# Performance work log

Hardware: AMD Instinct MI355X
Metric: run time of the kernel (lower is better)

## Reference

```python
import jax, jax.numpy as jnp
import numpy as np

N_NODES = 10000
N_EDGES = 160000
D = 42          # node_input_dim == node_hidden_dim
DE = 10         # edge_input_dim
DEH = 42        # edge_hidden_dim
N_STEPS = 6


def setup_inputs() -> dict:
    key = jax.random.key(0)
    ks = jax.random.split(key, 16)
    s = 0.1
    return {
        "n_feat": jax.random.normal(ks[0], (N_NODES, D), jnp.float32),
        "e_feat": jax.random.normal(ks[1], (N_EDGES, DE), jnp.float32),
        "src": jax.random.randint(ks[2], (N_EDGES,), 0, N_NODES),
        "dst": jax.random.randint(ks[3], (N_EDGES,), 0, N_NODES),
        # lin0: node_input_dim -> node_hidden_dim
        "lin0_w": s * jax.random.normal(ks[4], (D, D), jnp.float32),
        "lin0_b": s * jax.random.normal(ks[5], (D,), jnp.float32),
        # message_layer: hidden -> hidden
        "msg_w": s * jax.random.normal(ks[6], (D, D), jnp.float32),
        "msg_b": s * jax.random.normal(ks[7], (D,), jnp.float32),
        # edge_network: Linear(10,42) -> ReLU -> Linear(42, 42*42)
        "en_w1": s * jax.random.normal(ks[8], (DE, DEH), jnp.float32),
        "en_b1": s * jax.random.normal(ks[9], (DEH,), jnp.float32),
        "en_w2": s * jax.random.normal(ks[10], (DEH, D * D), jnp.float32),
        "en_b2": s * jax.random.normal(ks[11], (D * D,), jnp.float32),
        # NNConv bias (DGL NNConv has bias=True by default)
        "conv_b": s * jax.random.normal(ks[12], (D,), jnp.float32),
    }


def reference(n_feat, e_feat, src, dst,
              lin0_w, lin0_b, msg_w, msg_b,
              en_w1, en_b1, en_w2, en_b2, conv_b):
    N, d = n_feat.shape
    init = n_feat
    out = jax.nn.relu(n_feat @ lin0_w + lin0_b)                      # [N, d]
    # Per-edge weight matrices from edge features (e_feat is constant
    # across steps, so the edge MLP is hoisted out of the loop).
    w_edge = (jax.nn.relu(e_feat @ en_w1 + en_b1) @ en_w2 + en_b2)   # [E, d*d]
    w_edge = w_edge.reshape(-1, d, d)                                # [E, d_in, d_out]
    for _ in range(N_STEPS):
        # NNConv: gather src feats, per-edge matvec, scatter-sum to dst
        msgs = jnp.einsum('ei,eio->eo', out[src], w_edge)            # [E, d]
        agg = jax.ops.segment_sum(msgs, dst, num_segments=N)         # [N, d]
        # residual (in==out -> identity res_fc) + bias, then outer ReLU
        m = jax.nn.relu(agg + out + conv_b)
        out = jax.nn.relu(m @ msg_w + msg_b)
    return out + init
```

## Files before the change

### kernel.cpp

```cpp
#include <hip/hip_runtime.h>
#include <hip/hip_bf16.h>


#define N_NODES 10000
#define N_EDGES 160000
#define NCHK 5000
#define D 42
#define DE 10
#define XSTR 48
#define KI 1806
#define NKSTEP 57
#define SSTR 1832

typedef __attribute__((ext_vector_type(8))) short short8;
typedef __attribute__((ext_vector_type(4))) float f32x4;

__global__ __launch_bounds__(256) void k_lin0(const float* __restrict__ nf,
        const float* __restrict__ w, const float* __restrict__ b,
        __hip_bfloat16* __restrict__ out16) {
    int idx = blockIdx.x * 256 + threadIdx.x;
    if (idx >= N_NODES * XSTR) return;
    int n = idx / XSTR, j = idx % XSTR;
    float v = 0.f;
    if (j < D) {
        const float* row = nf + n * D;
        float acc = b[j];
        #pragma unroll
        for (int i = 0; i < D; ++i) acc = fmaf(row[i], w[i * D + j], acc);
        v = fmaxf(acc, 0.f);
    }
    out16[idx] = __float2bfloat16(v);
}

__global__ __launch_bounds__(256) void k_T2B(const float* __restrict__ w2,
        const float* __restrict__ b2, __hip_bfloat16* __restrict__ Bfr) {
    int idx = blockIdx.x * 256 + threadIdx.x;
    if (idx >= 3 * NKSTEP * 64 * 8) return;
    int j = idx & 7, lane = (idx >> 3) & 63;
    int ks = (idx >> 9) % NKSTEP, nt = idx / (NKSTEP * 512);
    int col = nt * 16 + (lane & 15);
    int k = ks * 32 + ((lane >> 4) * 8) + j;
    float v = 0.f;
    if (col < D && k < KI) {
        int kk = k / D, ii = k % D;
        v = (kk < D) ? w2[kk * (D * D) + ii * D + col] : b2[ii * D + col];
    }
    Bfr[idx] = __float2bfloat16(v);
}

__global__ __launch_bounds__(256) void k_hist(const int* __restrict__ dst,
        int* __restrict__ cnt) {
    int e = blockIdx.x * 256 + threadIdx.x;
    if (e < N_EDGES) atomicAdd(&cnt[dst[e]], 1);
}

__global__ __launch_bounds__(1024) void k_scan(const int* __restrict__ cnt,
        int* __restrict__ row_ptr, int* __restrict__ cursor) {
    __shared__ int buf[1024];
    __shared__ int s_run;
    const int t = threadIdx.x;
    if (t == 0) s_run = 0;
    __syncthreads();
    for (int base = 0; base < N_NODES; base += 1024) {
        int v = (base + t < N_NODES) ? cnt[base + t] : 0;
        buf[t] = v;
        __syncthreads();
        for (int off = 1; off < 1024; off <<= 1) {
            int add = (t >= off) ? buf[t - off] : 0;
            __syncthreads();
            buf[t] += add;
            __syncthreads();
        }
        int excl = buf[t] - v;
        if (base + t < N_NODES) {
            int val = s_run + excl;
            row_ptr[base + t] = val;
            cursor[base + t]  = val;
        }
        __syncthreads();
        if (t == 0) s_run += buf[1023];
        __syncthreads();
    }
    if (t == 0) { row_ptr[N_NODES] = s_run; cursor[N_NODES] = s_run; }
}

__global__ __launch_bounds__(256) void k_scatter(const int* __restrict__ dst,
        const int* __restrict__ src, int* __restrict__ cursor,
        int* __restrict__ srcp, int* __restrict__ eperm) {
    int e = blockIdx.x * 256 + threadIdx.x;
    if (e < N_EDGES) {
        int p = atomicAdd(&cursor[dst[e]], 1);
        srcp[p] = src[e];
        eperm[p] = e;
    }
}

__global__ __launch_bounds__(256) void k_hT(const float* __restrict__ ef,
        const float* __restrict__ w1, const float* __restrict__ b1,
        const int* __restrict__ eperm, __hip_bfloat16* __restrict__ hpT) {
    const int c = blockIdx.x;
    const int t = threadIdx.x;
    for (int j = t; j < 48 * 32; j += 256) {
        int k = j >> 5, ep = j & 31;
        int e = eperm[c * 32 + ep];
        float v;
        if (k < D) {
            const float* row = ef + (size_t)e * DE;
            float acc = b1[k];
            #pragma unroll
            for (int i = 0; i < DE; ++i) acc = fmaf(row[i], w1[i * D + k], acc);
            v = fmaxf(acc, 0.f);
        } else {
            v = (k == D) ? 1.0f : 0.f;
        }
        hpT[(size_t)c * 1536 + j] = __float2bfloat16(v);
    }
}

#define MFMA(A, B, C) C = __builtin_amdgcn_mfma_f32_16x16x32_bf16(A, B, C, 0, 0, 0)

__global__ __launch_bounds__(256) void k_step3(
        const __hip_bfloat16* __restrict__ hpT,
        const __hip_bfloat16* __restrict__ out_in,
        const int* __restrict__ srcp, const int* __restrict__ row_ptr,
        const __hip_bfloat16* __restrict__ Bfr,
        const float* __restrict__ nf, const float* __restrict__ msg_w,
        const float* __restrict__ msg_b, const float* __restrict__ conv_b,
        __hip_bfloat16* __restrict__ out16_dst, float* __restrict__ fout,
        int last) {
    __shared__ __align__(16) __hip_bfloat16 sS[8 * SSTR];
    __shared__ float sR[8 * 48];
    __shared__ float sM[8 * 48];
    const int t = threadIdx.x;
    const int wv = t >> 6;
    const int l = t & 63;
    const int g = l >> 4;
    const int g8 = g * 8;
    const int cl = l & 15;
    const int n0 = blockIdx.x * 8;
    const short* hpTs = (const short*)hpT;
    const short* xs = (const short*)out_in;

    for (int i = t; i < 8 * 48; i += 256) sR[i] = 0.f;
    for (int i = t; i < 8 * 18; i += 256)
        sS[(i / 18) * SSTR + KI + (i % 18)] = __float2bfloat16(0.f);

    const int nodeA = n0 + wv * 2, nodeB = nodeA + 1;
    const int begA = row_ptr[nodeA], endA = row_ptr[nodeA + 1];
    const int begB = endA, endB = row_ptr[nodeB + 1];
    const int c0A = begA >> 5, ncA = (endA > begA) ? ((endA - 1) >> 5) - c0A + 1 : 0;
    const int c0B = begB >> 5, ncB = (endB > begB) ? ((endB - 1) >> 5) - c0B + 1 : 0;
    const int ncmax = max(ncA, ncB);

    f32x4 cA[9], cB[9];
    #pragma unroll
    for (int i = 0; i < 9; ++i) { cA[i] = {0.f,0.f,0.f,0.f}; cB[i] = cA[i]; }

    for (int ci = 0; ci < ncmax; ++ci) {
        short8 aA0, aA1, aA2, bA0, bA1, bA2;
        short8 aB0, aB1, aB2, bB0, bB1, bB2;
        bool doA = ci < ncA, doB = ci < ncB;
        if (doA) {
            const int c = c0A + ci, c32 = c << 5;
            const short* hb = hpTs + (size_t)c * 1536 + cl * 32 + g8;
            aA0 = *(const short8*)(hb);
            aA1 = *(const short8*)(hb + 16 * 32);
            aA2 = *(const short8*)(hb + 32 * 32);
            int4 s0 = *(const int4*)(srcp + c32 + g8);
            int4 s1 = *(const int4*)(srcp + c32 + g8 + 4);
            const int se[8] = {s0.x, s0.y, s0.z, s0.w, s1.x, s1.y, s1.z, s1.w};
            #pragma unroll
            for (int j = 0; j < 8; ++j) {
                const short* xr = xs + (size_t)se[j] * XSTR + cl;
                bA0[j] = xr[0]; bA1[j] = xr[16]; bA2[j] = xr[32];
            }
            if (c32 < begA || c32 + 32 > endA) {
                #pragma unroll
                for (int j = 0; j < 8; ++j) {
                    int ep = c32 + g8 + j;
                    if (ep < begA || ep >= endA) { aA0[j] = 0; aA1[j] = 0; aA2[j] = 0; }
                }
            }
        }
        if (doB) {
            const int c = c0B + ci, c32 = c << 5;
            const short* hb = hpTs + (size_t)c * 1536 + cl * 32 + g8;
            aB0 = *(const short8*)(hb);
            aB1 = *(const short8*)(hb + 16 * 32);
            aB2 = *(const short8*)(hb + 32 * 32);
            int4 s0 = *(const int4*)(srcp + c32 + g8);
            int4 s1 = *(const int4*)(srcp + c32 + g8 + 4);
            const int se[8] = {s0.x, s0.y, s0.z, s0.w, s1.x, s1.y, s1.z, s1.w};
            #pragma unroll
            for (int j = 0; j < 8; ++j) {
                const short* xr = xs + (size_t)se[j] * XSTR + cl;
                bB0[j] = xr[0]; bB1[j] = xr[16]; bB2[j] = xr[32];
            }
            if (c32 < begB || c32 + 32 > endB) {
                #pragma unroll
                for (int j = 0; j < 8; ++j) {
                    int ep = c32 + g8 + j;
                    if (ep < begB || ep >= endB) { aB0[j] = 0; aB1[j] = 0; aB2[j] = 0; }
                }
            }
        }
        if (doA) {
            MFMA(aA0, bA0, cA[0]); MFMA(aA0, bA1, cA[1]); MFMA(aA0, bA2, cA[2]);
            MFMA(aA1, bA0, cA[3]); MFMA(aA1, bA1, cA[4]); MFMA(aA1, bA2, cA[5]);
            MFMA(aA2, bA0, cA[6]); MFMA(aA2, bA1, cA[7]); MFMA(aA2, bA2, cA[8]);
        }
        if (doB) {
            MFMA(aB0, bB0, cB[0]); MFMA(aB0, bB1, cB[1]); MFMA(aB0, bB2, cB[2]);
            MFMA(aB1, bB0, cB[3]); MFMA(aB1, bB1, cB[4]); MFMA(aB1, bB2, cB[5]);
            MFMA(aB2, bB0, cB[6]); MFMA(aB2, bB1, cB[7]); MFMA(aB2, bB2, cB[8]);
        }
    }
    #define ST(CC, NLOC, MT, NT)                                             \
        _Pragma("unroll")                                                    \
        for (int r = 0; r < 4; ++r) {                                        \
            int m = (MT) * 16 + g * 4 + r;                                   \
            int col = (NT) * 16 + cl;                                        \
            if (m < 43 && col < D)                                           \
                sS[(NLOC) * SSTR + m * D + col] = __float2bfloat16(CC[r]);   \
        }
    {
        const int nlA = wv * 2, nlB = nlA + 1;
        ST(cA[0], nlA, 0, 0) ST(cA[1], nlA, 0, 1) ST(cA[2], nlA, 0, 2)
        ST(cA[3], nlA, 1, 0) ST(cA[4], nlA, 1, 1) ST(cA[5], nlA, 1, 2)
        ST(cA[6], nlA, 2, 0) ST(cA[7], nlA, 2, 1) ST(cA[8], nlA, 2, 2)
        ST(cB[0], nlB, 0, 0) ST(cB[1], nlB, 0, 1) ST(cB[2], nlB, 0, 2)
        ST(cB[3], nlB, 1, 0) ST(cB[4], nlB, 1, 1) ST(cB[5], nlB, 1, 2)
        ST(cB[6], nlB, 2, 0) ST(cB[7], nlB, 2, 1) ST(cB[8], nlB, 2, 2)
    }
    #undef ST
    __syncthreads();

    {
        const int ks0 = (wv == 0) ? 0 : (wv * 14 + 1);
        const int ks1 = wv * 14 + 15;
        f32x4 d0 = {0.f,0.f,0.f,0.f}, d1 = d0, d2 = d0;
        const short* sSrow = (const short*)sS + (cl & 7) * SSTR + g8;
        const short* bb = (const short*)Bfr + (size_t)l * 8;
        for (int ks = ks0; ks < ks1; ++ks) {
            short8 a  = *(const short8*)(sSrow + ks * 32);
            short8 B0 = *(const short8*)(bb + (size_t)(0 * NKSTEP + ks) * 512);
            short8 B1 = *(const short8*)(bb + (size_t)(1 * NKSTEP + ks) * 512);
            short8 B2 = *(const short8*)(bb + (size_t)(2 * NKSTEP + ks) * 512);
            MFMA(a, B0, d0); MFMA(a, B1, d1); MFMA(a, B2, d2);
        }
        if (g < 2) {
            const int rl = g * 4;
            #pragma unroll
            for (int r = 0; r < 4; ++r) {
                atomicAdd(&sR[(rl + r) * 48 + cl],      d0[r]);
                atomicAdd(&sR[(rl + r) * 48 + 16 + cl], d1[r]);
                atomicAdd(&sR[(rl + r) * 48 + 32 + cl], d2[r]);
            }
        }
    }
    __syncthreads();

    float* sW = (float*)sS;
    for (int i = t; i < D * D; i += 256) sW[i] = msg_w[i];
    for (int idx = t; idx < 8 * 48; idx += 256) {
        int nl_ = idx / 48, o = idx % 48;
        float mv = 0.f;
        if (o < D) {
            float res = __bfloat162float(out_in[(size_t)(n0 + nl_) * XSTR + o]);
            mv = fmaxf(sR[idx] + res + conv_b[o], 0.f);
        }
        sM[idx] = mv;
    }
    __syncthreads();

    for (int idx = t; idx < 8 * 48; idx += 256) {
        int nl_ = idx / 48, pcol = idx % 48;
        if (pcol < D) {
            float s = msg_b[pcol];
            #pragma unroll 6
            for (int o = 0; o < D; ++o)
                s = fmaf(sM[nl_ * 48 + o], sW[o * D + pcol], s);
            float v = fmaxf(s, 0.f);
            if (last) {
                fout[(size_t)(n0 + nl_) * D + pcol] =
                    v + nf[(size_t)(n0 + nl_) * D + pcol];
            } else {
                out16_dst[(size_t)(n0 + nl_) * XSTR + pcol] = __float2bfloat16(v);
            }
        } else if (!last) {
            out16_dst[(size_t)(n0 + nl_) * XSTR + pcol] = __float2bfloat16(0.f);
        }
    }
}

extern "C" void kernel_launch(void* const* d_in, const int* in_sizes, int n_in,
                              void* d_out, int out_size, void* d_ws, size_t ws_size,
                              hipStream_t stream) {
    const float* nf    = (const float*)d_in[0];
    const float* ef    = (const float*)d_in[1];
    const int*   src   = (const int*)d_in[2];
    const int*   dst   = (const int*)d_in[3];
    const float* lin0w = (const float*)d_in[4];
    const float* lin0b = (const float*)d_in[5];
    const float* msgw  = (const float*)d_in[6];
    const float* msgb  = (const float*)d_in[7];
    const float* enw1  = (const float*)d_in[8];
    const float* enb1  = (const float*)d_in[9];
    const float* enw2  = (const float*)d_in[10];
    const float* enb2  = (const float*)d_in[11];
    const float* convb = (const float*)d_in[12];

    char* p = (char*)d_ws;
    auto alloc = [&](size_t bytes) -> char* {
        char* r = p; p += (bytes + 255) & ~(size_t)255; return r;
    };
    __hip_bfloat16* outA = (__hip_bfloat16*)alloc((size_t)N_NODES * XSTR * 2);
    __hip_bfloat16* outB = (__hip_bfloat16*)alloc((size_t)N_NODES * XSTR * 2);
    __hip_bfloat16* hpT  = (__hip_bfloat16*)alloc((size_t)NCHK * 1536 * 2);
    __hip_bfloat16* Bfr  = (__hip_bfloat16*)alloc((size_t)3 * NKSTEP * 64 * 8 * 2);
    int* cnt    = (int*)alloc((N_NODES + 1) * 4);
    int* rowp   = (int*)alloc((N_NODES + 1) * 4);
    int* cur    = (int*)alloc((N_NODES + 1) * 4);
    int* srcp   = (int*)alloc((size_t)N_EDGES * 4);
    int* eperm  = (int*)alloc((size_t)N_EDGES * 4);

    hipMemsetAsync(cnt, 0, (N_NODES + 1) * 4, stream);
    k_lin0<<<(N_NODES * XSTR + 255) / 256, 256, 0, stream>>>(nf, lin0w, lin0b, outA);
    k_T2B<<<(3 * NKSTEP * 64 * 8 + 255) / 256, 256, 0, stream>>>(enw2, enb2, Bfr);
    k_hist<<<(N_EDGES + 255) / 256, 256, 0, stream>>>(dst, cnt);
    k_scan<<<1, 1024, 0, stream>>>(cnt, rowp, cur);
    k_scatter<<<(N_EDGES + 255) / 256, 256, 0, stream>>>(dst, src, cur, srcp, eperm);
    k_hT<<<NCHK, 256, 0, stream>>>(ef, enw1, enb1, eperm, hpT);

    const int tiles = N_NODES / 8;
    __hip_bfloat16* bufs[2] = {outA, outB};
    for (int s_i = 0; s_i < 6; ++s_i) {
        const __hip_bfloat16* cin = bufs[s_i % 2];
        __hip_bfloat16* cout = bufs[(s_i + 1) % 2];
        int last = (s_i == 5) ? 1 : 0;
        k_step3<<<tiles, 256, 0, stream>>>(hpT, cin, srcp, rowp, Bfr,
                                           nf, msgw, msgb, convb,
                                           cout, (float*)d_out, last);
    }
}
```

Before: 357.9 us.

## Pre-gather source features into transposed chunk layout and enlarge node tiles

Adds a per-step k_gx kernel that gathers source-node features by edge order into a chunked transposed bf16 buffer (xeT), so the main step kernel loads B operands with contiguous vector loads instead of per-element scattered gathers. The step kernel now uses 512 threads and 16 nodes per block, handles one node at a time per wave with software prefetch of the next chunk, and uses all 16 MFMA rows in the second contraction. This trades an extra kernel launch and an extra round trip through global memory each step for coalesced loads and better MFMA utilisation.

```diff
diff --git a/kernel.cpp b/kernel.cpp
--- a/kernel.cpp
+++ b/kernel.cpp
@@ -117,129 +117,123 @@
     }
 }
 
+__global__ __launch_bounds__(256) void k_gx(
+        const __hip_bfloat16* __restrict__ x16, const int* __restrict__ srcp,
+        __hip_bfloat16* __restrict__ xeT) {
+    __shared__ short sx[128][50];
+    const int t = threadIdx.x;
+    const int base = blockIdx.x * 128;
+    const short* xs = (const short*)x16;
+    for (int idx = t; idx < 128 * 6; idx += 256) {
+        int el = idx / 6, cs = idx % 6;
+        int sp = srcp[base + el];
+        *(short8*)&sx[el][cs * 8] = *(const short8*)(xs + (size_t)sp * XSTR + cs * 8);
+    }
+    __syncthreads();
+    short* out = (short*)xeT + (size_t)blockIdx.x * 4 * 1536;
+    for (int idx = t; idx < 768; idx += 256) {
+        int cc = idx / 192, rem = idx % 192, row = rem >> 2, h8 = rem & 3;
+        short8 v;
+        #pragma unroll
+        for (int j = 0; j < 8; ++j) v[j] = sx[cc * 32 + h8 * 8 + j][row];
+        *(short8*)(out + (size_t)cc * 1536 + row * 32 + h8 * 8) = v;
+    }
+}
+
 #define MFMA(A, B, C) C = __builtin_amdgcn_mfma_f32_16x16x32_bf16(A, B, C, 0, 0, 0)
 
-__global__ __launch_bounds__(256) void k_step3(
+__global__ __launch_bounds__(512, 4) void k_step4(
         const __hip_bfloat16* __restrict__ hpT,
+        const __hip_bfloat16* __restrict__ xeT,
         const __hip_bfloat16* __restrict__ out_in,
-        const int* __restrict__ srcp, const int* __restrict__ row_ptr,
+        const int* __restrict__ row_ptr,
         const __hip_bfloat16* __restrict__ Bfr,
         const float* __restrict__ nf, const float* __restrict__ msg_w,
         const float* __restrict__ msg_b, const float* __restrict__ conv_b,
         __hip_bfloat16* __restrict__ out16_dst, float* __restrict__ fout,
         int last) {
-    __shared__ __align__(16) __hip_bfloat16 sS[8 * SSTR];
-    __shared__ float sR[8 * 48];
-    __shared__ float sM[8 * 48];
+    __shared__ __align__(16) __hip_bfloat16 sS[16 * SSTR];
+    __shared__ float sR[16 * 48];
+    __shared__ float sM[16 * 48];
     const int t = threadIdx.x;
     const int wv = t >> 6;
     const int l = t & 63;
     const int g = l >> 4;
     const int g8 = g * 8;
     const int cl = l & 15;
-    const int n0 = blockIdx.x * 8;
+    const int n0 = blockIdx.x * 16;
     const short* hpTs = (const short*)hpT;
-    const short* xs = (const short*)out_in;
-
-    for (int i = t; i < 8 * 48; i += 256) sR[i] = 0.f;
-    for (int i = t; i < 8 * 18; i += 256)
+    const short* xeTs = (const short*)xeT;
+
+    for (int i = t; i < 16 * 48; i += 512) sR[i] = 0.f;
+    for (int i = t; i < 16 * 18; i += 512)
         sS[(i / 18) * SSTR + KI + (i % 18)] = __float2bfloat16(0.f);
 
-    const int nodeA = n0 + wv * 2, nodeB = nodeA + 1;
-    const int begA = row_ptr[nodeA], endA = row_ptr[nodeA + 1];
-    const int begB = endA, endB = row_ptr[nodeB + 1];
-    const int c0A = begA >> 5, ncA = (endA > begA) ? ((endA - 1) >> 5) - c0A + 1 : 0;
-    const int c0B = begB >> 5, ncB = (endB > begB) ? ((endB - 1) >> 5) - c0B + 1 : 0;
-    const int ncmax = max(ncA, ncB);
-
-    f32x4 cA[9], cB[9];
-    #pragma unroll
-    for (int i = 0; i < 9; ++i) { cA[i] = {0.f,0.f,0.f,0.f}; cB[i] = cA[i]; }
-
-    for (int ci = 0; ci < ncmax; ++ci) {
-        short8 aA0, aA1, aA2, bA0, bA1, bA2;
-        short8 aB0, aB1, aB2, bB0, bB1, bB2;
-        bool doA = ci < ncA, doB = ci < ncB;
-        if (doA) {
-            const int c = c0A + ci, c32 = c << 5;
-            const short* hb = hpTs + (size_t)c * 1536 + cl * 32 + g8;
-            aA0 = *(const short8*)(hb);
-            aA1 = *(const short8*)(hb + 16 * 32);
-            aA2 = *(const short8*)(hb + 32 * 32);
-            int4 s0 = *(const int4*)(srcp + c32 + g8);
-            int4 s1 = *(const int4*)(srcp + c32 + g8 + 4);
-            const int se[8] = {s0.x, s0.y, s0.z, s0.w, s1.x, s1.y, s1.z, s1.w};
-            #pragma unroll
-            for (int j = 0; j < 8; ++j) {
-                const short* xr = xs + (size_t)se[j] * XSTR + cl;
-                bA0[j] = xr[0]; bA1[j] = xr[16]; bA2[j] = xr[32];
+    for (int q = 0; q < 2; ++q) {
+        const int nloc = wv * 2 + q;
+        const int node = n0 + nloc;
+        const int beg = row_ptr[node], end = row_ptr[node + 1];
+        const int c0 = beg >> 5;
+        const int nc = (end > beg) ? ((end - 1) >> 5) - c0 + 1 : 0;
+
+        f32x4 cc[9];
+        #pragma unroll
+        for (int i = 0; i < 9; ++i) cc[i] = {0.f, 0.f, 0.f, 0.f};
+
+        short8 a0, a1, a2, b0, b1, b2;
+        if (nc > 0) {
+            const size_t hb = (size_t)c0 * 1536 + cl * 32 + g8;
+            a0 = *(const short8*)(hpTs + hb);
+            a1 = *(const short8*)(hpTs + hb + 512);
+            a2 = *(const short8*)(hpTs + hb + 1024);
+            b0 = *(const short8*)(xeTs + hb);
+            b1 = *(const short8*)(xeTs + hb + 512);
+            b2 = *(const short8*)(xeTs + hb + 1024);
+        }
+        for (int ci = 0; ci < nc; ++ci) {
+            short8 na0, na1, na2, nb0, nb1, nb2;
+            if (ci + 1 < nc) {
+                const size_t hb = (size_t)(c0 + ci + 1) * 1536 + cl * 32 + g8;
+                na0 = *(const short8*)(hpTs + hb);
+                na1 = *(const short8*)(hpTs + hb + 512);
+                na2 = *(const short8*)(hpTs + hb + 1024);
+                nb0 = *(const short8*)(xeTs + hb);
+                nb1 = *(const short8*)(xeTs + hb + 512);
+                nb2 = *(const short8*)(xeTs + hb + 1024);
             }
-            if (c32 < begA || c32 + 32 > endA) {
+            const int c32 = (c0 + ci) << 5;
+            if (c32 < beg || c32 + 32 > end) {
                 #pragma unroll
                 for (int j = 0; j < 8; ++j) {
                     int ep = c32 + g8 + j;
-                    if (ep < begA || ep >= endA) { aA0[j] = 0; aA1[j] = 0; aA2[j] = 0; }
+                    if (ep < beg || ep >= end) { a0[j] = 0; a1[j] = 0; a2[j] = 0; }
                 }
             }
-        }
-        if (doB) {
-            const int c = c0B + ci, c32 = c << 5;
-            const short* hb = hpTs + (size_t)c * 1536 + cl * 32 + g8;
-            aB0 = *(const short8*)(hb);
-            aB1 = *(const short8*)(hb + 16 * 32);
-            aB2 = *(const short8*)(hb + 32 * 32);
-            int4 s0 = *(const int4*)(srcp + c32 + g8);
-            int4 s1 = *(const int4*)(srcp + c32 + g8 + 4);
-            const int se[8] = {s0.x, s0.y, s0.z, s0.w, s1.x, s1.y, s1.z, s1.w};
-            #pragma unroll
-            for (int j = 0; j < 8; ++j) {
-                const short* xr = xs + (size_t)se[j] * XSTR + cl;
-                bB0[j] = xr[0]; bB1[j] = xr[16]; bB2[j] = xr[32];
+            MFMA(a0, b0, cc[0]); MFMA(a0, b1, cc[1]); MFMA(a0, b2, cc[2]);
+            MFMA(a1, b0, cc[3]); MFMA(a1, b1, cc[4]); MFMA(a1, b2, cc[5]);
+            MFMA(a2, b0, cc[6]); MFMA(a2, b1, cc[7]); MFMA(a2, b2, cc[8]);
+            a0 = na0; a1 = na1; a2 = na2; b0 = nb0; b1 = nb1; b2 = nb2;
+        }
+        #define ST(CI, MT, NT)                                               \
+            _Pragma("unroll")                                                \
+            for (int r = 0; r < 4; ++r) {                                    \
+                int m = (MT) * 16 + g * 4 + r;                               \
+                int col = (NT) * 16 + cl;                                    \
+                if (m < 43 && col < D)                                       \
+                    sS[nloc * SSTR + m * D + col] = __float2bfloat16(cc[CI][r]); \
             }
-            if (c32 < begB || c32 + 32 > endB) {
-                #pragma unroll
-                for (int j = 0; j < 8; ++j) {
-                    int ep = c32 + g8 + j;
-                    if (ep < begB || ep >= endB) { aB0[j] = 0; aB1[j] = 0; aB2[j] = 0; }
-                }
-            }
-        }
-        if (doA) {
-            MFMA(aA0, bA0, cA[0]); MFMA(aA0, bA1, cA[1]); MFMA(aA0, bA2, cA[2]);
-            MFMA(aA1, bA0, cA[3]); MFMA(aA1, bA1, cA[4]); MFMA(aA1, bA2, cA[5]);
-            MFMA(aA2, bA0, cA[6]); MFMA(aA2, bA1, cA[7]); MFMA(aA2, bA2, cA[8]);
-        }
-        if (doB) {
-            MFMA(aB0, bB0, cB[0]); MFMA(aB0, bB1, cB[1]); MFMA(aB0, bB2, cB[2]);
-            MFMA(aB1, bB0, cB[3]); MFMA(aB1, bB1, cB[4]); MFMA(aB1, bB2, cB[5]);
-            MFMA(aB2, bB0, cB[6]); MFMA(aB2, bB1, cB[7]); MFMA(aB2, bB2, cB[8]);
-        }
-    }
-    #define ST(CC, NLOC, MT, NT)                                             \
-        _Pragma("unroll")                                                    \
-        for (int r = 0; r < 4; ++r) {                                        \
-            int m = (MT) * 16 + g * 4 + r;                                   \
-            int col = (NT) * 16 + cl;                                        \
-            if (m < 43 && col < D)                                           \
-                sS[(NLOC) * SSTR + m * D + col] = __float2bfloat16(CC[r]);   \
-        }
+        ST(0, 0, 0) ST(1, 0, 1) ST(2, 0, 2)
+        ST(3, 1, 0) ST(4, 1, 1) ST(5, 1, 2)
+        ST(6, 2, 0) ST(7, 2, 1) ST(8, 2, 2)
+        #undef ST
+    }
+    __syncthreads();
+
     {
-        const int nlA = wv * 2, nlB = nlA + 1;
-        ST(cA[0], nlA, 0, 0) ST(cA[1], nlA, 0, 1) ST(cA[2], nlA, 0, 2)
-        ST(cA[3], nlA, 1, 0) ST(cA[4], nlA, 1, 1) ST(cA[5], nlA, 1, 2)
-        ST(cA[6], nlA, 2, 0) ST(cA[7], nlA, 2, 1) ST(cA[8], nlA, 2, 2)
-        ST(cB[0], nlB, 0, 0) ST(cB[1], nlB, 0, 1) ST(cB[2], nlB, 0, 2)
-        ST(cB[3], nlB, 1, 0) ST(cB[4], nlB, 1, 1) ST(cB[5], nlB, 1, 2)
-        ST(cB[6], nlB, 2, 0) ST(cB[7], nlB, 2, 1) ST(cB[8], nlB, 2, 2)
-    }
-    #undef ST
-    __syncthreads();
-
-    {
-        const int ks0 = (wv == 0) ? 0 : (wv * 14 + 1);
-        const int ks1 = wv * 14 + 15;
-        f32x4 d0 = {0.f,0.f,0.f,0.f}, d1 = d0, d2 = d0;
-        const short* sSrow = (const short*)sS + (cl & 7) * SSTR + g8;
+        const int ks0 = (wv == 0) ? 0 : (wv * 7 + 1);
+        const int ks1 = wv * 7 + 8;
+        f32x4 d0 = {0.f, 0.f, 0.f, 0.f}, d1 = d0, d2 = d0;
+        const short* sSrow = (const short*)sS + cl * SSTR + g8;
         const short* bb = (const short*)Bfr + (size_t)l * 8;
         for (int ks = ks0; ks < ks1; ++ks) {
             short8 a  = *(const short8*)(sSrow + ks * 32);
@@ -248,21 +242,19 @@
             short8 B2 = *(const short8*)(bb + (size_t)(2 * NKSTEP + ks) * 512);
             MFMA(a, B0, d0); MFMA(a, B1, d1); MFMA(a, B2, d2);
         }
-        if (g < 2) {
-            const int rl = g * 4;
-            #pragma unroll
-            for (int r = 0; r < 4; ++r) {
-                atomicAdd(&sR[(rl + r) * 48 + cl],      d0[r]);
-                atomicAdd(&sR[(rl + r) * 48 + 16 + cl], d1[r]);
-                atomicAdd(&sR[(rl + r) * 48 + 32 + cl], d2[r]);
-            }
+        const int rl = g * 4;
+        #pragma unroll
+        for (int r = 0; r < 4; ++r) {
+            atomicAdd(&sR[(rl + r) * 48 + cl],      d0[r]);
+            atomicAdd(&sR[(rl + r) * 48 + 16 + cl], d1[r]);
+            atomicAdd(&sR[(rl + r) * 48 + 32 + cl], d2[r]);
         }
     }
     __syncthreads();
 
     float* sW = (float*)sS;
-    for (int i = t; i < D * D; i += 256) sW[i] = msg_w[i];
-    for (int idx = t; idx < 8 * 48; idx += 256) {
+    for (int i = t; i < D * D; i += 512) sW[i] = msg_w[i];
+    for (int idx = t; idx < 16 * 48; idx += 512) {
         int nl_ = idx / 48, o = idx % 48;
         float mv = 0.f;
         if (o < D) {
@@ -273,7 +265,7 @@
     }
     __syncthreads();
 
-    for (int idx = t; idx < 8 * 48; idx += 256) {
+    for (int idx = t; idx < 16 * 48; idx += 512) {
         int nl_ = idx / 48, pcol = idx % 48;
         if (pcol < D) {
             float s = msg_b[pcol];
@@ -317,6 +309,7 @@
     __hip_bfloat16* outA = (__hip_bfloat16*)alloc((size_t)N_NODES * XSTR * 2);
     __hip_bfloat16* outB = (__hip_bfloat16*)alloc((size_t)N_NODES * XSTR * 2);
     __hip_bfloat16* hpT  = (__hip_bfloat16*)alloc((size_t)NCHK * 1536 * 2);
+    __hip_bfloat16* xeT  = (__hip_bfloat16*)alloc((size_t)NCHK * 1536 * 2);
     __hip_bfloat16* Bfr  = (__hip_bfloat16*)alloc((size_t)3 * NKSTEP * 64 * 8 * 2);
     int* cnt    = (int*)alloc((N_NODES + 1) * 4);
     int* rowp   = (int*)alloc((N_NODES + 1) * 4);
@@ -332,13 +325,14 @@
     k_scatter<<<(N_EDGES + 255) / 256, 256, 0, stream>>>(dst, src, cur, srcp, eperm);
     k_hT<<<NCHK, 256, 0, stream>>>(ef, enw1, enb1, eperm, hpT);
 
-    const int tiles = N_NODES / 8;
+    const int tiles = N_NODES / 16;
     __hip_bfloat16* bufs[2] = {outA, outB};
     for (int s_i = 0; s_i < 6; ++s_i) {
         const __hip_bfloat16* cin = bufs[s_i % 2];
         __hip_bfloat16* cout = bufs[(s_i + 1) % 2];
         int last = (s_i == 5) ? 1 : 0;
-        k_step3<<<tiles, 256, 0, stream>>>(hpT, cin, srcp, rowp, Bfr,
+        k_gx<<<NCHK / 4, 256, 0, stream>>>(cin, srcp, xeT);
+        k_step4<<<tiles, 512, 0, stream>>>(hpT, xeT, cin, rowp, Bfr,
                                            nf, msgw, msgb, convb,
                                            cout, (float*)d_out, last);
     }
```

New measurement: 425.7 us. 19.0% more time.
